# Kernel tuning notes

Measured on AMD Instinct MI355X. Metric: run time of the kernel, lower is better.

Reference implementation:

```python
import jax, jax.numpy as jnp
import numpy as np

B, T, X, Y, H = 256, 1024, 64, 64, 256


def setup_inputs() -> dict:
    key = jax.random.key(0)
    ks = jax.random.split(key, 7)
    inputs = jax.random.normal(ks[0], (B, T, X + Y), dtype=jnp.float32)
    # zero out the last quarter of timesteps so Masking(mask_value=0.0) is exercised
    tmask = (jnp.arange(T) < (3 * T) // 4).astype(jnp.float32)[None, :, None]
    inputs = inputs * tmask
    s = 0.05
    return {
        "inputs": inputs,
        "W_enc": jax.random.normal(ks[1], (X + Y, 4 * H), dtype=jnp.float32) * s,
        "U_enc": jax.random.normal(ks[2], (H, 4 * H), dtype=jnp.float32) * s,
        "b_enc": jnp.zeros((4 * H,), dtype=jnp.float32),
        "W_dec": jax.random.normal(ks[3], (X + H, 4 * H), dtype=jnp.float32) * s,
        "U_dec": jax.random.normal(ks[4], (H, 4 * H), dtype=jnp.float32) * s,
        "b_dec": jnp.zeros((4 * H,), dtype=jnp.float32),
        "W_out": jax.random.normal(ks[5], (H, Y), dtype=jnp.float32) * s,
        "b_out": jnp.zeros((Y,), dtype=jnp.float32),
        "x_dim": X,
    }


def _lstm_relu(xW_t, U, mask_t=None, return_seq=False):
    """Keras LSTM with activation='relu', recurrent_activation='sigmoid'.
    xW_t: [T,B,4H] precomputed x@W + b. mask_t: optional [T,B] bool.
    Gate order i, f, c, o (Keras). Masked steps carry (h, c) through.
    """
    Hn = U.shape[0]
    Bn = xW_t.shape[1]
    h0 = jnp.zeros((Bn, Hn), dtype=xW_t.dtype)
    c0 = jnp.zeros((Bn, Hn), dtype=xW_t.dtype)

    def step(carry, inp):
        h, c = carry
        if mask_t is None:
            xw = inp
        else:
            xw, m = inp
        z = xw + h @ U                       # [B,4H]
        i, f, g, o = jnp.split(z, 4, axis=-1)
        i = jax.nn.sigmoid(i)
        f = jax.nn.sigmoid(f)
        o = jax.nn.sigmoid(o)
        g = jax.nn.relu(g)                   # activation='relu'
        c_new = f * c + i * g
        h_new = o * jax.nn.relu(c_new)       # activation='relu' on cell output
        if mask_t is not None:
            mm = m[:, None]
            h_new = jnp.where(mm, h_new, h)
            c_new = jnp.where(mm, c_new, c)
        return (h_new, c_new), (h_new if return_seq else None)

    xs = xW_t if mask_t is None else (xW_t, mask_t)
    (h_fin, _), hs = jax.lax.scan(step, (h0, c0), xs)
    return h_fin, hs


def reference(inputs, W_enc, U_enc, b_enc, W_dec, U_dec, b_dec, W_out, b_out, x_dim):
    # Masking(mask_value=0.0): timestep valid iff any feature != 0
    mask = jnp.any(inputs != 0.0, axis=-1)                 # [B,T]
    # Encoder LSTM, return_sequences=False
    xW = jnp.einsum('bti,ij->btj', inputs, W_enc) + b_enc  # [B,T,4H]
    h_fin, _ = _lstm_relu(xW.transpose(1, 0, 2), U_enc,
                          mask_t=mask.T, return_seq=False)  # [B,H]
    # RepeatVector + concat with x part
    Tn = inputs.shape[1]
    latent_rep = jnp.broadcast_to(h_fin[:, None, :], (h_fin.shape[0], Tn, h_fin.shape[1]))
    dec_inp = jnp.concatenate([inputs[:, :, :x_dim], latent_rep], axis=-1)  # [B,T,X+H]
    # Decoder LSTM, return_sequences=True (no mask)
    xW2 = jnp.einsum('bti,ij->btj', dec_inp, W_dec) + b_dec
    _, hs = _lstm_relu(xW2.transpose(1, 0, 2), U_dec, mask_t=None, return_seq=True)  # [T,B,H]
    hs = hs.transpose(1, 0, 2)                              # [B,T,H]
    # TimeDistributed Dense(y_dim)
    return jnp.einsum('bth,hy->bty', hs, W_out) + b_out
```

## Files before the change

kernel.cpp:

```cpp
#include <hip/hip_runtime.h>


typedef __bf16 bf16x8 __attribute__((ext_vector_type(8)));
typedef float f32x4 __attribute__((ext_vector_type(4)));
typedef unsigned int uint4v __attribute__((ext_vector_type(4)));
typedef unsigned long long ull;

#define DI __device__ __forceinline__

DI unsigned short f2bf(float f) {
  unsigned int u = __float_as_uint(f);
  u += 0x7fffu + ((u >> 16) & 1u);
  return (unsigned short)(u >> 16);
}
DI float sigf(float v) { return 1.0f / (1.0f + __expf(-v)); }

DI void barrier_lds() {
  asm volatile("s_waitcnt lgkmcnt(0)\n\ts_barrier" ::: "memory");
}

union FragU { bf16x8 v; unsigned short us[8]; };
union H8 { bf16x8 v; ull u[2]; uint4v q; };

DI f32x4 mfma16(bf16x8 a, bf16x8 b, f32x4 c) {
  return __builtin_amdgcn_mfma_f32_16x16x32_bf16(a, b, c, 0, 0, 0);
}
DI ull ald(const ull* p) {
  return __hip_atomic_load(p, __ATOMIC_RELAXED, __HIP_MEMORY_SCOPE_AGENT);
}

__global__ void pack_frags(const float* __restrict__ src,
                           unsigned short* __restrict__ dst, int K, int N) {
  int KT = K >> 5, NT = N >> 4;
  int total = KT * NT * 64;
  for (int idx = blockIdx.x * blockDim.x + threadIdx.x; idx < total;
       idx += gridDim.x * blockDim.x) {
    int lane = idx & 63;
    int fi = idx >> 6;
    int nt = fi % NT;
    int kt = fi / NT;
    int r0 = kt * 32 + (lane >> 4) * 8;
    int col = nt * 16 + (lane & 15);
    unsigned int w[4];
#pragma unroll
    for (int p = 0; p < 4; ++p) {
      unsigned int lo = f2bf(src[(size_t)(r0 + 2 * p) * N + col]);
      unsigned int hi = f2bf(src[(size_t)(r0 + 2 * p + 1) * N + col]);
      w[p] = lo | (hi << 16);
    }
    *(uint4v*)(dst + (size_t)idx * 8) = (uint4v){w[0], w[1], w[2], w[3]};
  }
}

__global__ void mask_flags(const float* __restrict__ x,
                           unsigned int* __restrict__ fmask) {
  const int t = blockIdx.x;
  const int b = threadIdx.x;
  const float* p = x + ((size_t)b * 1024 + t) * 128;
  bool nz = false;
#pragma unroll 8
  for (int k = 0; k < 32; ++k) {
    float4 v = *(const float4*)(p + k * 4);
    nz = nz || v.x != 0.f || v.y != 0.f || v.z != 0.f || v.w != 0.f;
  }
  unsigned long long bal = __ballot((int)nz);
  if ((threadIdx.x & 15) == 0)
    fmask[(size_t)(b >> 4) * 1024 + t] =
        (unsigned int)((bal >> (threadIdx.x & 48)) & 0xFFFFull);
}

#define STORE_OWN(HX, PAR, TAG) do {                                        \
    if (tid < 128) {                                                        \
      const int kth = tid >> 6, word = tid & 63;                            \
      H8 hh; hh.q = *(const uint4v*)&hstage[2 * s + kth][word][0];          \
      const ull tg = (ull)(TAG);                                            \
      ull Aw = (hh.u[0] & 0xFFFFFFFFFFFFULL) | (tg << 48);                  \
      ull Bw = ((hh.u[0] >> 48) | ((hh.u[1] & 0xFFFFFFFFULL) << 16)) |      \
               (tg << 48);                                                  \
      ull Cw = (hh.u[1] >> 32) | (tg << 48);                                \
      ull* p_ = (HX) + (size_t)(g * 2 + (PAR)) * 1536 +                     \
                ((2 * s + kth) * 64 + word) * 3;                            \
      __hip_atomic_store(p_ + 0, Aw, __ATOMIC_RELAXED, __HIP_MEMORY_SCOPE_AGENT); \
      __hip_atomic_store(p_ + 1, Bw, __ATOMIC_RELAXED, __HIP_MEMORY_SCOPE_AGENT); \
      __hip_atomic_store(p_ + 2, Cw, __ATOMIC_RELAXED, __HIP_MEMORY_SCOPE_AGENT); \
    } } while (0)

#define POLL_REMOTE(HX, PAR, TAG) do {                                      \
    if (w >= 1) {                                                           \
      const int s2_ = (w - 1) + ((w - 1) >= s ? 1 : 0);                     \
      const int rk0 = 2 * s2_, rk1 = rk0 + 1;                               \
      const ull* hb_ = (HX) + (size_t)(g * 2 + (PAR)) * 1536;               \
      const ull* q0 = hb_ + (rk0 * 64 + lane) * 3;                          \
      const ull* q1 = hb_ + (rk1 * 64 + lane) * 3;                          \
      const ull tg = (ull)(TAG);                                            \
      ull A0, A1, A2, B0, B1, B2;                                           \
      unsigned it_ = 0;                                                     \
      for (;;) {                                                            \
        A0 = ald(q0); A1 = ald(q0 + 1); A2 = ald(q0 + 2);                   \
        B0 = ald(q1); B1 = ald(q1 + 1); B2 = ald(q1 + 2);                   \
        bool ok_ = ((A0 >> 48) == tg) && ((A1 >> 48) == tg) &&              \
                   ((A2 >> 48) == tg) && ((B0 >> 48) == tg) &&              \
                   ((B1 >> 48) == tg) && ((B2 >> 48) == tg);                \
        if (ok_ || ++it_ > (1u << 14)) break;                               \
      }                                                                     \
      H8 h0_, h1_;                                                          \
      h0_.u[0] = (A0 & 0xFFFFFFFFFFFFULL) | (A1 << 48);                     \
      h0_.u[1] = ((A1 >> 16) & 0xFFFFFFFFULL) | ((A2 & 0xFFFFFFFFULL) << 32); \
      h1_.u[0] = (B0 & 0xFFFFFFFFFFFFULL) | (B1 << 48);                     \
      h1_.u[1] = ((B1 >> 16) & 0xFFFFFFFFULL) | ((B2 & 0xFFFFFFFFULL) << 32); \
      *(uint4v*)&hstage[rk0][lane][0] = h0_.q;                              \
      *(uint4v*)&hstage[rk1][lane][0] = h1_.q;                              \
    } } while (0)

__global__ __launch_bounds__(256) __attribute__((amdgpu_waves_per_eu(1, 1)))
void enc_rnn(const float* __restrict__ x,
             const unsigned short* __restrict__ Wef,
             const unsigned short* __restrict__ Uef,
             const float* __restrict__ benc,
             const unsigned int* __restrict__ fmask,
             ull* __restrict__ hxE,
             unsigned short* __restrict__ hfin) {
  __shared__ __align__(16) unsigned short hstage[8][64][8];

  const int tid = threadIdx.x;
  const int w = tid >> 6, lane = tid & 63;
  const int l15 = lane & 15, lkg = lane >> 4;
  const int bid = blockIdx.x;
  const int s = bid >> 4, g = bid & 15;
  const int b0 = g * 16;
  int ntf[4];
#pragma unroll
  for (int G = 0; G < 4; ++G) ntf[G] = G * 16 + s * 4 + w;

  const bf16x8* Wl = (const bf16x8*)Wef + lane;
  const bf16x8* Ul = (const bf16x8*)Uef + lane;
  const unsigned int* flagp = fmask + (size_t)g * 1024;

  bf16x8 upin[8][4];
#pragma unroll
  for (int kt = 0; kt < 8; ++kt)
#pragma unroll
    for (int G = 0; G < 4; ++G) upin[kt][G] = Ul[(kt * 64 + ntf[G]) * 64];

  bf16x8 wpin[4][4];
#pragma unroll
  for (int G = 0; G < 4; ++G)
#pragma unroll
    for (int kt = 0; kt < 4; ++kt) wpin[G][kt] = Wl[(kt * 64 + ntf[G]) * 64];

  float bfr[4];
#pragma unroll
  for (int G = 0; G < 4; ++G) bfr[G] = benc[ntf[G] * 16 + l15];

  float c4[4];
  unsigned short hreg[4];
  bf16x8 hfr[8];
#pragma unroll
  for (int q = 0; q < 4; ++q) { c4[q] = 0.f; hreg[q] = 0; }
  H8 z_; z_.u[0] = 0; z_.u[1] = 0;
#pragma unroll
  for (int kt = 0; kt < 8; ++kt) hfr[kt] = z_.v;

  const float* xbase = x + (size_t)(b0 + l15) * 1024 * 128 + lkg * 8;
  const int kt_own = 2 * s + (w >> 1);
  const int lbase = (w & 1) * 32 + (l15 >> 3) * 16 + lkg * 4;
  const int jst = l15 & 7;
  int a = 0;
  bool xvalid = false;
  float4 xa[4][2];

  __syncthreads();

  for (int t = 0; t < 1024; ++t) {
    const unsigned int flag_t = flagp[t];
    if (flag_t == 0u) { xvalid = false; continue; }

    if (!xvalid) {
      const float* xp = xbase + (size_t)t * 128;
#pragma unroll
      for (int kt = 0; kt < 4; ++kt) {
        xa[kt][0] = *(const float4*)(xp + kt * 32);
        xa[kt][1] = *(const float4*)(xp + kt * 32 + 4);
      }
    }

    f32x4 acc[4];
#pragma unroll
    for (int G = 0; G < 4; ++G) acc[G] = (f32x4){bfr[G], bfr[G], bfr[G], bfr[G]};

    FragU xf[4];
#pragma unroll
    for (int kt = 0; kt < 4; ++kt) {
      xf[kt].us[0] = f2bf(xa[kt][0].x); xf[kt].us[1] = f2bf(xa[kt][0].y);
      xf[kt].us[2] = f2bf(xa[kt][0].z); xf[kt].us[3] = f2bf(xa[kt][0].w);
      xf[kt].us[4] = f2bf(xa[kt][1].x); xf[kt].us[5] = f2bf(xa[kt][1].y);
      xf[kt].us[6] = f2bf(xa[kt][1].z); xf[kt].us[7] = f2bf(xa[kt][1].w);
    }
#pragma unroll
    for (int kt = 0; kt < 4; ++kt)
#pragma unroll
      for (int G = 0; G < 4; ++G) acc[G] = mfma16(xf[kt].v, wpin[G][kt], acc[G]);

#pragma unroll
    for (int kt = 0; kt < 8; ++kt)
#pragma unroll
      for (int G = 0; G < 4; ++G) acc[G] = mfma16(hfr[kt], upin[kt][G], acc[G]);

    unsigned short hv[4];
#pragma unroll
    for (int q = 0; q < 4; ++q) {
      float iv = sigf(acc[0][q]);
      float fv = sigf(acc[1][q]);
      float gv = fmaxf(acc[2][q], 0.f);
      float ov = sigf(acc[3][q]);
      float cn = fv * c4[q] + iv * gv;
      float hn = ov * fmaxf(cn, 0.f);
      bool m = (flag_t >> (lkg * 4 + q)) & 1u;
      c4[q] = m ? cn : c4[q];
      unsigned short hh = m ? f2bf(hn) : hreg[q];
      hreg[q] = hh;
      hv[q] = hh;
    }

    barrier_lds();
#pragma unroll
    for (int q = 0; q < 4; ++q) hstage[kt_own][lbase + q][jst] = hv[q];
    barrier_lds();

    STORE_OWN(hxE, (a & 1), a + 1);

    if (t < 1023) {
      const float* xq = xbase + (size_t)(t + 1) * 128;
#pragma unroll
      for (int kt = 0; kt < 4; ++kt) {
        xa[kt][0] = *(const float4*)(xq + kt * 32);
        xa[kt][1] = *(const float4*)(xq + kt * 32 + 4);
      }
      xvalid = true;
    } else xvalid = false;

    POLL_REMOTE(hxE, (a & 1), a + 1);
    barrier_lds();

#pragma unroll
    for (int kt = 0; kt < 8; ++kt)
      hfr[kt] = *(const bf16x8*)&hstage[kt][lane][0];
    ++a;
  }

  if (w < 2) {
    int kt = 2 * s + w;
    H8 hh_; hh_.v = hfr[kt];
    *(uint4v*)&hfin[((size_t)g * 8 + kt) * 512 + lane * 8] = hh_.q;
  }
}

__global__ __launch_bounds__(256) __attribute__((amdgpu_waves_per_eu(1, 1)))
void dec_rnn(const float* __restrict__ x,
             const unsigned short* __restrict__ Wd0f,
             const unsigned short* __restrict__ WdLf,
             const unsigned short* __restrict__ Udf,
             const float* __restrict__ bdec,
             const unsigned short* __restrict__ Wof,
             const float* __restrict__ bout,
             const unsigned short* __restrict__ hfin,
             ull* __restrict__ hxD,
             float* __restrict__ out) {
  __shared__ __align__(16) unsigned short hstage[8][64][8];

  const int tid = threadIdx.x;
  const int w = tid >> 6, lane = tid & 63;
  const int l15 = lane & 15, lkg = lane >> 4;
  const int bid = blockIdx.x;
  const int s = bid >> 4, g = bid & 15;
  const int b0 = g * 16;
  int ntf[4];
#pragma unroll
  for (int G = 0; G < 4; ++G) ntf[G] = G * 16 + s * 4 + w;

  const bf16x8* W0l = (const bf16x8*)Wd0f + lane;
  const bf16x8* WLl = (const bf16x8*)WdLf + lane;
  const bf16x8* Ul  = (const bf16x8*)Udf + lane;

  bf16x8 upin[8][4];
#pragma unroll
  for (int kt = 0; kt < 8; ++kt)
#pragma unroll
    for (int G = 0; G < 4; ++G) upin[kt][G] = Ul[(kt * 64 + ntf[G]) * 64];

  bf16x8 w0pin[4][2];
#pragma unroll
  for (int G = 0; G < 4; ++G)
#pragma unroll
    for (int kt = 0; kt < 2; ++kt) w0pin[G][kt] = W0l[(kt * 64 + ntf[G]) * 64];

  f32x4 lat[4];
  {
    bf16x8 ha[8];
#pragma unroll
    for (int kt = 0; kt < 8; ++kt)
      ha[kt] = *(const bf16x8*)&hfin[((size_t)g * 8 + kt) * 512 + lane * 8];
#pragma unroll
    for (int G = 0; G < 4; ++G) {
      float bd = bdec[ntf[G] * 16 + l15];
      lat[G] = (f32x4){bd, bd, bd, bd};
    }
#pragma unroll
    for (int kt = 0; kt < 8; ++kt)
#pragma unroll
      for (int G = 0; G < 4; ++G)
        lat[G] = mfma16(ha[kt], WLl[(kt * 64 + ntf[G]) * 64], lat[G]);
  }

  bf16x8 wofr[8];
  if (w == 0) {
#pragma unroll
    for (int kt = 0; kt < 8; ++kt)
      wofr[kt] = ((const bf16x8*)Wof)[(kt * 4 + s) * 64 + lane];
  }
  const float bo = bout[s * 16 + l15];

  float c4[4];
  bf16x8 hfr[8];
#pragma unroll
  for (int q = 0; q < 4; ++q) c4[q] = 0.f;
  H8 z_; z_.u[0] = 0; z_.u[1] = 0;
#pragma unroll
  for (int kt = 0; kt < 8; ++kt) hfr[kt] = z_.v;

  const float* xbase = x + (size_t)(b0 + l15) * 1024 * 128 + lkg * 8;
  const int kt_own = 2 * s + (w >> 1);
  const int lbase = (w & 1) * 32 + (l15 >> 3) * 16 + lkg * 4;
  const int jst = l15 & 7;

  float4 xa[2][2];
  xa[0][0] = *(const float4*)(xbase);      xa[0][1] = *(const float4*)(xbase + 4);
  xa[1][0] = *(const float4*)(xbase + 32); xa[1][1] = *(const float4*)(xbase + 36);

  __syncthreads();

  for (int t = 0; t < 1024; ++t) {
    f32x4 acc[4];
#pragma unroll
    for (int G = 0; G < 4; ++G) acc[G] = lat[G];

    FragU xf[2];
#pragma unroll
    for (int kt = 0; kt < 2; ++kt) {
      xf[kt].us[0] = f2bf(xa[kt][0].x); xf[kt].us[1] = f2bf(xa[kt][0].y);
      xf[kt].us[2] = f2bf(xa[kt][0].z); xf[kt].us[3] = f2bf(xa[kt][0].w);
      xf[kt].us[4] = f2bf(xa[kt][1].x); xf[kt].us[5] = f2bf(xa[kt][1].y);
      xf[kt].us[6] = f2bf(xa[kt][1].z); xf[kt].us[7] = f2bf(xa[kt][1].w);
    }
#pragma unroll
    for (int kt = 0; kt < 2; ++kt)
#pragma unroll
      for (int G = 0; G < 4; ++G) acc[G] = mfma16(xf[kt].v, w0pin[G][kt], acc[G]);

#pragma unroll
    for (int kt = 0; kt < 8; ++kt)
#pragma unroll
      for (int G = 0; G < 4; ++G) acc[G] = mfma16(hfr[kt], upin[kt][G], acc[G]);

    unsigned short hv[4];
#pragma unroll
    for (int q = 0; q < 4; ++q) {
      float iv = sigf(acc[0][q]);
      float fv = sigf(acc[1][q]);
      float gv = fmaxf(acc[2][q], 0.f);
      float ov = sigf(acc[3][q]);
      float cn = fv * c4[q] + iv * gv;
      float hn = ov * fmaxf(cn, 0.f);
      c4[q] = cn;
      hv[q] = f2bf(hn);
    }

    barrier_lds();
#pragma unroll
    for (int q = 0; q < 4; ++q) hstage[kt_own][lbase + q][jst] = hv[q];
    barrier_lds();

    STORE_OWN(hxD, (t & 1), t + 1);

    if (t > 0 && w == 0) {
      f32x4 oa = {bo, bo, bo, bo};
#pragma unroll
      for (int kt = 0; kt < 8; ++kt) oa = mfma16(hfr[kt], wofr[kt], oa);
#pragma unroll
      for (int q = 0; q < 4; ++q)
        out[((size_t)(b0 + lkg * 4 + q) * 1024 + (t - 1)) * 64 + s * 16 + l15] = oa[q];
    }
    if (t < 1023) {
      const float* xq = xbase + (size_t)(t + 1) * 128;
      xa[0][0] = *(const float4*)(xq);      xa[0][1] = *(const float4*)(xq + 4);
      xa[1][0] = *(const float4*)(xq + 32); xa[1][1] = *(const float4*)(xq + 36);
    }

    POLL_REMOTE(hxD, (t & 1), t + 1);
    barrier_lds();

#pragma unroll
    for (int kt = 0; kt < 8; ++kt)
      hfr[kt] = *(const bf16x8*)&hstage[kt][lane][0];
  }

  if (w == 0) {
    f32x4 oa = {bo, bo, bo, bo};
#pragma unroll
    for (int kt = 0; kt < 8; ++kt) oa = mfma16(hfr[kt], wofr[kt], oa);
#pragma unroll
    for (int q = 0; q < 4; ++q)
      out[((size_t)(b0 + lkg * 4 + q) * 1024 + 1023) * 64 + s * 16 + l15] = oa[q];
  }
}

extern "C" void kernel_launch(void* const* d_in, const int* in_sizes, int n_in,
                              void* d_out, int out_size, void* d_ws, size_t ws_size,
                              hipStream_t stream) {
  const float* inputs = (const float*)d_in[0];
  const float* W_enc  = (const float*)d_in[1];
  const float* U_enc  = (const float*)d_in[2];
  const float* b_enc  = (const float*)d_in[3];
  const float* W_dec  = (const float*)d_in[4];
  const float* U_dec  = (const float*)d_in[5];
  const float* b_dec  = (const float*)d_in[6];
  const float* W_out  = (const float*)d_in[7];
  const float* b_out  = (const float*)d_in[8];

  char* ws = (char*)d_ws;
  unsigned short* Uef   = (unsigned short*)(ws + 0);
  unsigned short* Udf   = (unsigned short*)(ws + 524288);
  unsigned short* Wef   = (unsigned short*)(ws + 1048576);
  unsigned short* Wd0f  = (unsigned short*)(ws + 1310720);
  unsigned short* WdLf  = (unsigned short*)(ws + 1441792);
  unsigned short* Wof   = (unsigned short*)(ws + 1966080);
  unsigned short* hfin  = (unsigned short*)(ws + 1998848);
  unsigned int*   fmask = (unsigned int*)(ws + 2129920);
  ull*            hxE   = (ull*)(ws + 2195456);
  ull*            hxD   = (ull*)(ws + 2588672);

  mask_flags<<<1024, 256, 0, stream>>>(inputs, fmask);
  pack_frags<<<128, 256, 0, stream>>>(U_enc, Uef, 256, 1024);
  pack_frags<<<128, 256, 0, stream>>>(U_dec, Udf, 256, 1024);
  pack_frags<<<128, 256, 0, stream>>>(W_enc, Wef, 128, 1024);
  pack_frags<<<128, 256, 0, stream>>>(W_dec, Wd0f, 64, 1024);
  pack_frags<<<128, 256, 0, stream>>>(W_dec + 64 * 1024, WdLf, 256, 1024);
  pack_frags<<<32, 256, 0, stream>>>(W_out, Wof, 256, 64);

  enc_rnn<<<64, 256, 0, stream>>>(inputs, Wef, Uef, b_enc, fmask, hxE, hfin);
  dec_rnn<<<64, 256, 0, stream>>>(inputs, Wd0f, WdLf, Udf, b_dec, Wof, b_out,
                                  hfin, hxD, (float*)d_out);
}
```

Baseline: 5.291 ms.

## Double-issue polling loads in cross-block spin-wait and use __syncthreads barriers

The remote hidden-state poll now keeps two sets of atomic loads in flight, checking one set while the next is already issued, so each spin iteration overlaps load latency. The custom inline-asm LDS barrier is replaced with __syncthreads, which gives the compiler full knowledge of the barrier semantics and may let it schedule waits better. The extra speculative loads add memory traffic while spinning, and __syncthreads may add a wait on outstanding global memory (vmcnt) that the old lgkmcnt-only barrier avoided.

```diff
diff --git a/kernel.cpp b/kernel.cpp
--- a/kernel.cpp
+++ b/kernel.cpp
@@ -14,10 +14,6 @@
   return (unsigned short)(u >> 16);
 }
 DI float sigf(float v) { return 1.0f / (1.0f + __expf(-v)); }
-
-DI void barrier_lds() {
-  asm volatile("s_waitcnt lgkmcnt(0)\n\ts_barrier" ::: "memory");
-}
 
 union FragU { bf16x8 v; unsigned short us[8]; };
 union H8 { bf16x8 v; ull u[2]; uint4v q; };
@@ -93,21 +89,25 @@
       const ull* q0 = hb_ + (rk0 * 64 + lane) * 3;                          \
       const ull* q1 = hb_ + (rk1 * 64 + lane) * 3;                          \
       const ull tg = (ull)(TAG);                                            \
-      ull A0, A1, A2, B0, B1, B2;                                           \
+      ull A0 = ald(q0), A1 = ald(q0 + 1), A2 = ald(q0 + 2),                 \
+          A3 = ald(q1), A4 = ald(q1 + 1), A5 = ald(q1 + 2);                 \
+      ull B0 = ald(q0), B1 = ald(q0 + 1), B2 = ald(q0 + 2),                 \
+          B3 = ald(q1), B4 = ald(q1 + 1), B5 = ald(q1 + 2);                 \
       unsigned it_ = 0;                                                     \
       for (;;) {                                                            \
-        A0 = ald(q0); A1 = ald(q0 + 1); A2 = ald(q0 + 2);                   \
-        B0 = ald(q1); B1 = ald(q1 + 1); B2 = ald(q1 + 2);                   \
         bool ok_ = ((A0 >> 48) == tg) && ((A1 >> 48) == tg) &&              \
-                   ((A2 >> 48) == tg) && ((B0 >> 48) == tg) &&              \
-                   ((B1 >> 48) == tg) && ((B2 >> 48) == tg);                \
+                   ((A2 >> 48) == tg) && ((A3 >> 48) == tg) &&              \
+                   ((A4 >> 48) == tg) && ((A5 >> 48) == tg);                \
         if (ok_ || ++it_ > (1u << 14)) break;                               \
+        A0 = B0; A1 = B1; A2 = B2; A3 = B3; A4 = B4; A5 = B5;               \
+        B0 = ald(q0); B1 = ald(q0 + 1); B2 = ald(q0 + 2);                   \
+        B3 = ald(q1); B4 = ald(q1 + 1); B5 = ald(q1 + 2);                   \
       }                                                                     \
       H8 h0_, h1_;                                                          \
       h0_.u[0] = (A0 & 0xFFFFFFFFFFFFULL) | (A1 << 48);                     \
       h0_.u[1] = ((A1 >> 16) & 0xFFFFFFFFULL) | ((A2 & 0xFFFFFFFFULL) << 32); \
-      h1_.u[0] = (B0 & 0xFFFFFFFFFFFFULL) | (B1 << 48);                     \
-      h1_.u[1] = ((B1 >> 16) & 0xFFFFFFFFULL) | ((B2 & 0xFFFFFFFFULL) << 32); \
+      h1_.u[0] = (A3 & 0xFFFFFFFFFFFFULL) | (A4 << 48);                     \
+      h1_.u[1] = ((A4 >> 16) & 0xFFFFFFFFULL) | ((A5 & 0xFFFFFFFFULL) << 32); \
       *(uint4v*)&hstage[rk0][lane][0] = h0_.q;                              \
       *(uint4v*)&hstage[rk1][lane][0] = h1_.q;                              \
     } } while (0)
@@ -222,10 +222,10 @@
       hv[q] = hh;
     }
 
-    barrier_lds();
+    __syncthreads();
 #pragma unroll
     for (int q = 0; q < 4; ++q) hstage[kt_own][lbase + q][jst] = hv[q];
-    barrier_lds();
+    __syncthreads();
 
     STORE_OWN(hxE, (a & 1), a + 1);
 
@@ -240,7 +240,7 @@
     } else xvalid = false;
 
     POLL_REMOTE(hxE, (a & 1), a + 1);
-    barrier_lds();
+    __syncthreads();
 
 #pragma unroll
     for (int kt = 0; kt < 8; ++kt)
@@ -375,10 +375,10 @@
       hv[q] = f2bf(hn);
     }
 
-    barrier_lds();
+    __syncthreads();
 #pragma unroll
     for (int q = 0; q < 4; ++q) hstage[kt_own][lbase + q][jst] = hv[q];
-    barrier_lds();
+    __syncthreads();
 
     STORE_OWN(hxD, (t & 1), t + 1);
 
@@ -397,7 +397,7 @@
     }
 
     POLL_REMOTE(hxD, (t & 1), t + 1);
-    barrier_lds();
+    __syncthreads();
 
 #pragma unroll
     for (int kt = 0; kt < 8; ++kt)
```

After: 6.040 ms. 1.14x slower.

## Split RNN into chunked input GEMM, per-group step kernels, and output GEMM

Applied to the files above, without the earlier changes.

Replaces the 64-block cross-CU recurrent kernels, which exchange h through global atomics and polling, with a chunked pipeline. A parallel GEMM precomputes x@W (+bias/latent) for TC timesteps. A 16-block step kernel then runs the recurrence for those steps, with each block owning one batch group, keeping U partly in LDS and partly in registers, and syncing only with __syncthreads. A separate GEMM computes the decoder output projection. Inter-block spin polling disappears, but each step now runs on only 16 CUs, and the chunking adds many kernel launches plus round trips of state and xW through global memory. The old kernels stay as a fallback when workspace is too small.

```diff
diff --git a/kernel.cpp b/kernel.cpp
--- a/kernel.cpp
+++ b/kernel.cpp
@@ -5,21 +5,18 @@
 typedef float f32x4 __attribute__((ext_vector_type(4)));
 typedef unsigned int uint4v __attribute__((ext_vector_type(4)));
 typedef unsigned long long ull;
+typedef unsigned short ushort;
 
 #define DI __device__ __forceinline__
 
-DI unsigned short f2bf(float f) {
+DI ushort f2bf(float f) {
   unsigned int u = __float_as_uint(f);
   u += 0x7fffu + ((u >> 16) & 1u);
-  return (unsigned short)(u >> 16);
+  return (ushort)(u >> 16);
 }
 DI float sigf(float v) { return 1.0f / (1.0f + __expf(-v)); }
 
-DI void barrier_lds() {
-  asm volatile("s_waitcnt lgkmcnt(0)\n\ts_barrier" ::: "memory");
-}
-
-union FragU { bf16x8 v; unsigned short us[8]; };
+union FragU { bf16x8 v; ushort us[8]; };
 union H8 { bf16x8 v; ull u[2]; uint4v q; };
 
 DI f32x4 mfma16(bf16x8 a, bf16x8 b, f32x4 c) {
@@ -30,7 +27,7 @@
 }
 
 __global__ void pack_frags(const float* __restrict__ src,
-                           unsigned short* __restrict__ dst, int K, int N) {
+                           ushort* __restrict__ dst, int K, int N) {
   int KT = K >> 5, NT = N >> 4;
   int total = KT * NT * 64;
   for (int idx = blockIdx.x * blockDim.x + threadIdx.x; idx < total;
@@ -68,6 +65,315 @@
     fmask[(size_t)(b >> 4) * 1024 + t] =
         (unsigned int)((bal >> (threadIdx.x & 48)) & 0xFFFFull);
 }
+
+
+__global__ void bias_frag(const float* __restrict__ bias,
+                          float* __restrict__ latE) {
+  for (int idx = threadIdx.x; idx < 64 * 64; idx += blockDim.x) {
+    int nt = idx >> 6, lane = idx & 63;
+    float v = bias[nt * 16 + (lane & 15)];
+    f32x4 o = {v, v, v, v};
+    *(f32x4*)(latE + (size_t)idx * 4) = o;
+  }
+}
+
+__global__ void lat_dec(const ushort* __restrict__ hfin,
+                        const ushort* __restrict__ WdLf,
+                        const float* __restrict__ bdec,
+                        float* __restrict__ latD) {
+  const int g = blockIdx.x;
+  const int tid = threadIdx.x;
+  const int wv = tid >> 6, lane = tid & 63, l15 = lane & 15;
+  const bf16x8* WLl = (const bf16x8*)WdLf + lane;
+  bf16x8 ha[8];
+#pragma unroll
+  for (int kt = 0; kt < 8; ++kt)
+    ha[kt] = *(const bf16x8*)&hfin[((size_t)g * 8 + kt) * 512 + lane * 8];
+#pragma unroll
+  for (int j = 0; j < 16; ++j) {
+    int nt = wv * 16 + j;
+    float bd = bdec[nt * 16 + l15];
+    f32x4 acc = {bd, bd, bd, bd};
+#pragma unroll
+    for (int kt = 0; kt < 8; ++kt)
+      acc = mfma16(ha[kt], WLl[(kt * 64 + nt) * 64], acc);
+    *(f32x4*)(latD + ((size_t)g * 64 + nt) * 256 + lane * 4) = acc;
+  }
+}
+
+template <int NKT>
+__global__ void xw_gemm(const float* __restrict__ x,
+                        const ushort* __restrict__ Bf,
+                        const float* __restrict__ latf, int latGstride,
+                        float* __restrict__ xwbuf, int t0) {
+  const int tg = blockIdx.x;
+  const int trel = tg >> 4, g = tg & 15;
+  const int t = t0 + trel;
+  const int tid = threadIdx.x;
+  const int wv = tid >> 6, lane = tid & 63;
+  const int l15 = lane & 15, lkg = lane >> 4;
+
+  const float* xp = x + ((size_t)(g * 16 + l15) * 1024 + t) * 128 + lkg * 8;
+  FragU xf[NKT];
+#pragma unroll
+  for (int kt = 0; kt < NKT; ++kt) {
+    float4 a = *(const float4*)(xp + kt * 32);
+    float4 b = *(const float4*)(xp + kt * 32 + 4);
+    xf[kt].us[0] = f2bf(a.x); xf[kt].us[1] = f2bf(a.y);
+    xf[kt].us[2] = f2bf(a.z); xf[kt].us[3] = f2bf(a.w);
+    xf[kt].us[4] = f2bf(b.x); xf[kt].us[5] = f2bf(b.y);
+    xf[kt].us[6] = f2bf(b.z); xf[kt].us[7] = f2bf(b.w);
+  }
+  const bf16x8* Bl = (const bf16x8*)Bf + lane;
+  const float* latg = latf + (size_t)g * latGstride;
+  float* outb = xwbuf + (size_t)(trel * 16 + g) * 64 * 256;
+#pragma unroll
+  for (int j = 0; j < 16; ++j) {
+    int nt = wv * 16 + j;
+    f32x4 acc = *(const f32x4*)(latg + (size_t)nt * 256 + lane * 4);
+#pragma unroll
+    for (int kt = 0; kt < NKT; ++kt)
+      acc = mfma16(xf[kt].v, Bl[(kt * 64 + nt) * 64], acc);
+    *(f32x4*)(outb + (size_t)nt * 256 + lane * 4) = acc;
+  }
+}
+
+__global__ void out_gemm(const ushort* __restrict__ hchunk,
+                         const ushort* __restrict__ Wof,
+                         const float* __restrict__ bout,
+                         float* __restrict__ out, int t0) {
+  const int g = blockIdx.x & 15;
+  const int tq = blockIdx.x >> 4;
+  const int tid = threadIdx.x;
+  const int wv = tid >> 6, lane = tid & 63;
+  const int l15 = lane & 15, lkg = lane >> 4;
+  const int tc = tq * 4 + wv;
+  const int t = t0 + tc;
+
+  const ushort* hb = hchunk + (size_t)(tc * 16 + g) * 4096;
+  bf16x8 ha[8];
+#pragma unroll
+  for (int kt = 0; kt < 8; ++kt)
+    ha[kt] = *(const bf16x8*)&hb[kt * 512 + lane * 8];
+  const bf16x8* Wl = (const bf16x8*)Wof + lane;
+#pragma unroll
+  for (int nt = 0; nt < 4; ++nt) {
+    float bo = bout[nt * 16 + l15];
+    f32x4 acc = {bo, bo, bo, bo};
+#pragma unroll
+    for (int kt = 0; kt < 8; ++kt)
+      acc = mfma16(ha[kt], Wl[(kt * 4 + nt) * 64], acc);
+#pragma unroll
+    for (int q = 0; q < 4; ++q)
+      out[((size_t)(g * 16 + lkg * 4 + q) * 1024 + t) * 64 + nt * 16 + l15] =
+          acc[q];
+  }
+}
+
+
+__global__ __launch_bounds__(512) __attribute__((amdgpu_waves_per_eu(2, 2)))
+void enc_step(const float* __restrict__ xwbuf, const ushort* __restrict__ Uef,
+              const unsigned int* __restrict__ fmask,
+              float* __restrict__ cst, ushort* __restrict__ hst,
+              ushort* __restrict__ hfin, int t0, int TC, int first, int last) {
+  __shared__ __align__(16) ushort ulds[65536];
+  __shared__ __align__(16) ushort hstage[8][64][8];
+
+  const int tid = threadIdx.x;
+  const int w = tid >> 6, lane = tid & 63;
+  const int l15 = lane & 15, lkg = lane >> 4;
+  const int g = blockIdx.x;
+
+#pragma unroll
+  for (int k = 0; k < 16; ++k)
+    ((uint4v*)ulds)[tid + k * 512] = ((const uint4v*)Uef)[tid + k * 512];
+
+  const bf16x8* Ul = (const bf16x8*)Uef + lane;
+  bf16x8 upin[6][2][4];
+#pragma unroll
+  for (int k2 = 0; k2 < 6; ++k2)
+#pragma unroll
+    for (int P = 0; P < 2; ++P)
+#pragma unroll
+      for (int j = 0; j < 4; ++j)
+        upin[k2][P][j] = Ul[((k2 + 2) * 64 + j * 16 + 2 * w + P) * 64];
+
+  float c8[8];
+  ushort hreg[8];
+  if (first) {
+#pragma unroll
+    for (int i = 0; i < 8; ++i) { c8[i] = 0.f; hreg[i] = 0; }
+    ((uint4v*)hstage)[tid] = (uint4v){0u, 0u, 0u, 0u};
+  } else {
+#pragma unroll
+    for (int i = 0; i < 8; ++i) c8[i] = cst[((size_t)g * 512 + tid) * 8 + i];
+    ((uint4v*)hstage)[tid] = ((const uint4v*)hst)[g * 512 + tid];
+  }
+  __syncthreads();
+  if (!first) {
+#pragma unroll
+    for (int P = 0; P < 2; ++P)
+#pragma unroll
+      for (int q = 0; q < 4; ++q)
+        hreg[P * 4 + q] =
+            hstage[w][P * 32 + (l15 >> 3) * 16 + lkg * 4 + q][l15 & 7];
+  }
+
+  const unsigned int* flagp = fmask + (size_t)g * 1024 + t0;
+
+  for (int tc = 0; tc < TC; ++tc) {
+    const unsigned int flag = flagp[tc];
+    if (flag == 0u) continue;
+    const float* xwb = xwbuf + (size_t)(tc * 16 + g) * 64 * 256;
+    ushort hv[8];
+#pragma unroll
+    for (int P = 0; P < 2; ++P) {
+      const int cb = 2 * w + P;
+      f32x4 acc[4];
+#pragma unroll
+      for (int j = 0; j < 4; ++j)
+        acc[j] = *(const f32x4*)(xwb + (size_t)(j * 16 + cb) * 256 + lane * 4);
+#pragma unroll
+      for (int kt = 0; kt < 2; ++kt) {
+        bf16x8 h_ = *(const bf16x8*)&hstage[kt][lane][0];
+#pragma unroll
+        for (int j = 0; j < 4; ++j) {
+          bf16x8 u_ =
+              *(const bf16x8*)&ulds[((kt * 64 + j * 16 + cb) * 64 + lane) * 8];
+          acc[j] = mfma16(h_, u_, acc[j]);
+        }
+      }
+#pragma unroll
+      for (int kt = 2; kt < 8; ++kt) {
+        bf16x8 h_ = *(const bf16x8*)&hstage[kt][lane][0];
+#pragma unroll
+        for (int j = 0; j < 4; ++j)
+          acc[j] = mfma16(h_, upin[kt - 2][P][j], acc[j]);
+      }
+#pragma unroll
+      for (int q = 0; q < 4; ++q) {
+        float iv = sigf(acc[0][q]);
+        float fv = sigf(acc[1][q]);
+        float gv = fmaxf(acc[2][q], 0.f);
+        float ov = sigf(acc[3][q]);
+        float cn = fv * c8[P * 4 + q] + iv * gv;
+        float hn = ov * fmaxf(cn, 0.f);
+        bool m = (flag >> (lkg * 4 + q)) & 1u;
+        c8[P * 4 + q] = m ? cn : c8[P * 4 + q];
+        ushort hh = m ? f2bf(hn) : hreg[P * 4 + q];
+        hreg[P * 4 + q] = hh;
+        hv[P * 4 + q] = hh;
+      }
+    }
+    __syncthreads();
+#pragma unroll
+    for (int P = 0; P < 2; ++P)
+#pragma unroll
+      for (int q = 0; q < 4; ++q)
+        hstage[w][P * 32 + (l15 >> 3) * 16 + lkg * 4 + q][l15 & 7] =
+            hv[P * 4 + q];
+    __syncthreads();
+  }
+
+#pragma unroll
+  for (int i = 0; i < 8; ++i) cst[((size_t)g * 512 + tid) * 8 + i] = c8[i];
+  ((uint4v*)hst)[g * 512 + tid] = ((const uint4v*)hstage)[tid];
+  if (last) ((uint4v*)hfin)[g * 512 + tid] = ((const uint4v*)hstage)[tid];
+}
+
+__global__ __launch_bounds__(512) __attribute__((amdgpu_waves_per_eu(2, 2)))
+void dec_step(const float* __restrict__ xwbuf, const ushort* __restrict__ Udf,
+              float* __restrict__ cst, ushort* __restrict__ hst,
+              ushort* __restrict__ hchunk, int TC, int first) {
+  __shared__ __align__(16) ushort ulds[65536];
+  __shared__ __align__(16) ushort hstage[8][64][8];
+
+  const int tid = threadIdx.x;
+  const int w = tid >> 6, lane = tid & 63;
+  const int l15 = lane & 15, lkg = lane >> 4;
+  const int g = blockIdx.x;
+
+#pragma unroll
+  for (int k = 0; k < 16; ++k)
+    ((uint4v*)ulds)[tid + k * 512] = ((const uint4v*)Udf)[tid + k * 512];
+
+  const bf16x8* Ul = (const bf16x8*)Udf + lane;
+  bf16x8 upin[6][2][4];
+#pragma unroll
+  for (int k2 = 0; k2 < 6; ++k2)
+#pragma unroll
+    for (int P = 0; P < 2; ++P)
+#pragma unroll
+      for (int j = 0; j < 4; ++j)
+        upin[k2][P][j] = Ul[((k2 + 2) * 64 + j * 16 + 2 * w + P) * 64];
+
+  float c8[8];
+  if (first) {
+#pragma unroll
+    for (int i = 0; i < 8; ++i) c8[i] = 0.f;
+    ((uint4v*)hstage)[tid] = (uint4v){0u, 0u, 0u, 0u};
+  } else {
+#pragma unroll
+    for (int i = 0; i < 8; ++i) c8[i] = cst[((size_t)g * 512 + tid) * 8 + i];
+    ((uint4v*)hstage)[tid] = ((const uint4v*)hst)[g * 512 + tid];
+  }
+  __syncthreads();
+
+  for (int tc = 0; tc < TC; ++tc) {
+    const float* xwb = xwbuf + (size_t)(tc * 16 + g) * 64 * 256;
+    ushort hv[8];
+#pragma unroll
+    for (int P = 0; P < 2; ++P) {
+      const int cb = 2 * w + P;
+      f32x4 acc[4];
+#pragma unroll
+      for (int j = 0; j < 4; ++j)
+        acc[j] = *(const f32x4*)(xwb + (size_t)(j * 16 + cb) * 256 + lane * 4);
+#pragma unroll
+      for (int kt = 0; kt < 2; ++kt) {
+        bf16x8 h_ = *(const bf16x8*)&hstage[kt][lane][0];
+#pragma unroll
+        for (int j = 0; j < 4; ++j) {
+          bf16x8 u_ =
+              *(const bf16x8*)&ulds[((kt * 64 + j * 16 + cb) * 64 + lane) * 8];
+          acc[j] = mfma16(h_, u_, acc[j]);
+        }
+      }
+#pragma unroll
+      for (int kt = 2; kt < 8; ++kt) {
+        bf16x8 h_ = *(const bf16x8*)&hstage[kt][lane][0];
+#pragma unroll
+        for (int j = 0; j < 4; ++j)
+          acc[j] = mfma16(h_, upin[kt - 2][P][j], acc[j]);
+      }
+#pragma unroll
+      for (int q = 0; q < 4; ++q) {
+        float iv = sigf(acc[0][q]);
+        float fv = sigf(acc[1][q]);
+        float gv = fmaxf(acc[2][q], 0.f);
+        float ov = sigf(acc[3][q]);
+        float cn = fv * c8[P * 4 + q] + iv * gv;
+        c8[P * 4 + q] = cn;
+        hv[P * 4 + q] = f2bf(ov * fmaxf(cn, 0.f));
+      }
+    }
+    __syncthreads();
+#pragma unroll
+    for (int P = 0; P < 2; ++P)
+#pragma unroll
+      for (int q = 0; q < 4; ++q)
+        hstage[w][P * 32 + (l15 >> 3) * 16 + lkg * 4 + q][l15 & 7] =
+            hv[P * 4 + q];
+    __syncthreads();
+    ((uint4v*)hchunk)[(size_t)(tc * 16 + g) * 512 + tid] =
+        ((const uint4v*)hstage)[tid];
+  }
+
+#pragma unroll
+  for (int i = 0; i < 8; ++i) cst[((size_t)g * 512 + tid) * 8 + i] = c8[i];
+  ((uint4v*)hst)[g * 512 + tid] = ((const uint4v*)hstage)[tid];
+}
+
 
 #define STORE_OWN(HX, PAR, TAG) do {                                        \
     if (tid < 128) {                                                        \
@@ -114,13 +420,11 @@
 
 __global__ __launch_bounds__(256) __attribute__((amdgpu_waves_per_eu(1, 1)))
 void enc_rnn(const float* __restrict__ x,
-             const unsigned short* __restrict__ Wef,
-             const unsigned short* __restrict__ Uef,
+             const ushort* __restrict__ Wef, const ushort* __restrict__ Uef,
              const float* __restrict__ benc,
              const unsigned int* __restrict__ fmask,
-             ull* __restrict__ hxE,
-             unsigned short* __restrict__ hfin) {
-  __shared__ __align__(16) unsigned short hstage[8][64][8];
+             ull* __restrict__ hxE, ushort* __restrict__ hfin) {
+  __shared__ __align__(16) ushort hstage[8][64][8];
 
   const int tid = threadIdx.x;
   const int w = tid >> 6, lane = tid & 63;
@@ -153,7 +457,7 @@
   for (int G = 0; G < 4; ++G) bfr[G] = benc[ntf[G] * 16 + l15];
 
   float c4[4];
-  unsigned short hreg[4];
+  ushort hreg[4];
   bf16x8 hfr[8];
 #pragma unroll
   for (int q = 0; q < 4; ++q) { c4[q] = 0.f; hreg[q] = 0; }
@@ -206,7 +510,7 @@
 #pragma unroll
       for (int G = 0; G < 4; ++G) acc[G] = mfma16(hfr[kt], upin[kt][G], acc[G]);
 
-    unsigned short hv[4];
+    ushort hv[4];
 #pragma unroll
     for (int q = 0; q < 4; ++q) {
       float iv = sigf(acc[0][q]);
@@ -217,15 +521,15 @@
       float hn = ov * fmaxf(cn, 0.f);
       bool m = (flag_t >> (lkg * 4 + q)) & 1u;
       c4[q] = m ? cn : c4[q];
-      unsigned short hh = m ? f2bf(hn) : hreg[q];
+      ushort hh = m ? f2bf(hn) : hreg[q];
       hreg[q] = hh;
       hv[q] = hh;
     }
 
-    barrier_lds();
+    __syncthreads();
 #pragma unroll
     for (int q = 0; q < 4; ++q) hstage[kt_own][lbase + q][jst] = hv[q];
-    barrier_lds();
+    __syncthreads();
 
     STORE_OWN(hxE, (a & 1), a + 1);
 
@@ -240,7 +544,7 @@
     } else xvalid = false;
 
     POLL_REMOTE(hxE, (a & 1), a + 1);
-    barrier_lds();
+    __syncthreads();
 
 #pragma unroll
     for (int kt = 0; kt < 8; ++kt)
@@ -257,16 +561,12 @@
 
 __global__ __launch_bounds__(256) __attribute__((amdgpu_waves_per_eu(1, 1)))
 void dec_rnn(const float* __restrict__ x,
-             const unsigned short* __restrict__ Wd0f,
-             const unsigned short* __restrict__ WdLf,
-             const unsigned short* __restrict__ Udf,
-             const float* __restrict__ bdec,
-             const unsigned short* __restrict__ Wof,
-             const float* __restrict__ bout,
-             const unsigned short* __restrict__ hfin,
-             ull* __restrict__ hxD,
-             float* __restrict__ out) {
-  __shared__ __align__(16) unsigned short hstage[8][64][8];
+             const ushort* __restrict__ Wd0f, const ushort* __restrict__ WdLf,
+             const ushort* __restrict__ Udf,
+             const float* __restrict__ bdec, const ushort* __restrict__ Wof,
+             const float* __restrict__ bout, const ushort* __restrict__ hfin,
+             ull* __restrict__ hxD, float* __restrict__ out) {
+  __shared__ __align__(16) ushort hstage[8][64][8];
 
   const int tid = threadIdx.x;
   const int w = tid >> 6, lane = tid & 63;
@@ -362,7 +662,7 @@
 #pragma unroll
       for (int G = 0; G < 4; ++G) acc[G] = mfma16(hfr[kt], upin[kt][G], acc[G]);
 
-    unsigned short hv[4];
+    ushort hv[4];
 #pragma unroll
     for (int q = 0; q < 4; ++q) {
       float iv = sigf(acc[0][q]);
@@ -375,10 +675,10 @@
       hv[q] = f2bf(hn);
     }
 
-    barrier_lds();
+    __syncthreads();
 #pragma unroll
     for (int q = 0; q < 4; ++q) hstage[kt_own][lbase + q][jst] = hv[q];
-    barrier_lds();
+    __syncthreads();
 
     STORE_OWN(hxD, (t & 1), t + 1);
 
@@ -397,7 +697,7 @@
     }
 
     POLL_REMOTE(hxD, (t & 1), t + 1);
-    barrier_lds();
+    __syncthreads();
 
 #pragma unroll
     for (int kt = 0; kt < 8; ++kt)
@@ -428,16 +728,28 @@
   const float* b_out  = (const float*)d_in[8];
 
   char* ws = (char*)d_ws;
-  unsigned short* Uef   = (unsigned short*)(ws + 0);
-  unsigned short* Udf   = (unsigned short*)(ws + 524288);
-  unsigned short* Wef   = (unsigned short*)(ws + 1048576);
-  unsigned short* Wd0f  = (unsigned short*)(ws + 1310720);
-  unsigned short* WdLf  = (unsigned short*)(ws + 1441792);
-  unsigned short* Wof   = (unsigned short*)(ws + 1966080);
-  unsigned short* hfin  = (unsigned short*)(ws + 1998848);
-  unsigned int*   fmask = (unsigned int*)(ws + 2129920);
-  ull*            hxE   = (ull*)(ws + 2195456);
-  ull*            hxD   = (ull*)(ws + 2588672);
+  ushort* Uef   = (ushort*)(ws + 0);
+  ushort* Udf   = (ushort*)(ws + 524288);
+  ushort* Wef   = (ushort*)(ws + 1048576);
+  ushort* Wd0f  = (ushort*)(ws + 1310720);
+  ushort* WdLf  = (ushort*)(ws + 1441792);
+  ushort* Wof   = (ushort*)(ws + 1966080);
+  ushort* hfin  = (ushort*)(ws + 1998848);
+  unsigned int* fmask = (unsigned int*)(ws + 2129920);
+  ull*    hxE   = (ull*)(ws + 2195456);
+  ull*    hxD   = (ull*)(ws + 2588672);
+  float*  latE  = (float*)(ws + 2981888);
+  float*  latD  = (float*)(ws + 3047424);
+  float*  cstE  = (float*)(ws + 4096000);
+  ushort* hstE  = (ushort*)(ws + 4358144);
+  float*  cstD  = (float*)(ws + 4489216);
+  ushort* hstD  = (ushort*)(ws + 4751360);
+  const size_t base = 4882432;
+
+  int TC = 0;
+  if (ws_size >= base + (size_t)128 * (131072 + 1048576)) TC = 128;
+  else if (ws_size >= base + (size_t)64 * (131072 + 1048576)) TC = 64;
+  else if (ws_size >= base + (size_t)32 * (131072 + 1048576)) TC = 32;
 
   mask_flags<<<1024, 256, 0, stream>>>(inputs, fmask);
   pack_frags<<<128, 256, 0, stream>>>(U_enc, Uef, 256, 1024);
@@ -447,7 +759,30 @@
   pack_frags<<<128, 256, 0, stream>>>(W_dec + 64 * 1024, WdLf, 256, 1024);
   pack_frags<<<32, 256, 0, stream>>>(W_out, Wof, 256, 64);
 
-  enc_rnn<<<64, 256, 0, stream>>>(inputs, Wef, Uef, b_enc, fmask, hxE, hfin);
-  dec_rnn<<<64, 256, 0, stream>>>(inputs, Wd0f, WdLf, Udf, b_dec, Wof, b_out,
-                                  hfin, hxD, (float*)d_out);
-}
+  if (TC) {
+    ushort* hchunk = (ushort*)(ws + base);
+    float*  xwbuf  = (float*)(ws + base + (size_t)TC * 131072);
+    const int NC = 1024 / TC;
+
+    bias_frag<<<1, 256, 0, stream>>>(b_enc, latE);
+    for (int c = 0; c < NC; ++c) {
+      xw_gemm<4><<<TC * 16, 256, 0, stream>>>(inputs, Wef, latE, 0, xwbuf,
+                                              c * TC);
+      enc_step<<<16, 512, 0, stream>>>(xwbuf, Uef, fmask, cstE, hstE, hfin,
+                                       c * TC, TC, c == 0, c == NC - 1);
+    }
+    lat_dec<<<16, 256, 0, stream>>>(hfin, WdLf, b_dec, latD);
+    for (int c = 0; c < NC; ++c) {
+      xw_gemm<2><<<TC * 16, 256, 0, stream>>>(inputs, Wd0f, latD, 64 * 256,
+                                              xwbuf, c * TC);
+      dec_step<<<16, 512, 0, stream>>>(xwbuf, Udf, cstD, hstD, hchunk, TC,
+                                       c == 0);
+      out_gemm<<<16 * (TC / 4), 256, 0, stream>>>(hchunk, Wof, b_out,
+                                                  (float*)d_out, c * TC);
+    }
+  } else {
+    enc_rnn<<<64, 256, 0, stream>>>(inputs, Wef, Uef, b_enc, fmask, hxE, hfin);
+    dec_rnn<<<64, 256, 0, stream>>>(inputs, Wd0f, WdLf, Udf, b_dec, Wof, b_out,
+                                    hfin, hxD, (float*)d_out);
+  }
+}
```

Measured after the change: 9.679 ms. 1.83x slower.
